# Kernel optimization log

Measured on AMD Instinct MI355X. Metric: run time of the kernel, lower is better.

Reference implementation:

```python
import jax, jax.numpy as jnp
import numpy as np

EPS = 1e-3  # Keras BatchNormalization default epsilon


def _binarize(x):
    # sign() binarization with straight-through estimator (identity gradient)
    b = jnp.where(x >= 0, 1.0, -1.0).astype(x.dtype)
    return x + jax.lax.stop_gradient(b - x)


def _conv(x, w):
    # NHWC input, HWIO kernel, stride 1, 'same' padding
    return jax.lax.conv_general_dilated(
        x, w, (1, 1), 'SAME', dimension_numbers=('NHWC', 'HWIO', 'NHWC'))


def _bn(x, p):
    # p: [4, C] rows = gamma, beta, moving_mean, moving_var (inference BN)
    gamma, beta, mean, var = p[0], p[1], p[2], p[3]
    return gamma * (x - mean) * jax.lax.rsqrt(var + EPS) + beta


def _maxpool(x):
    return jax.lax.reduce_window(x, -jnp.inf, jax.lax.max,
                                 (1, 2, 2, 1), (1, 2, 2, 1), 'VALID')


def _bconv_block(x, w, bn_p):
    # BinaryConv2D(activation='relu', use_bias=False) -> BatchNormalization
    y = jax.nn.relu(_conv(_binarize(x), _binarize(w)))
    return _bn(y, bn_p)


def setup_inputs() -> dict:
    key = jax.random.key(0)
    ks = iter(jax.random.split(key, 64))

    def w(shape, scale=0.05):
        return jax.random.normal(next(ks), shape, jnp.float32) * scale

    def bn_params(c):
        gamma = 1.0 + 0.1 * jax.random.normal(next(ks), (c,), jnp.float32)
        beta = 0.1 * jax.random.normal(next(ks), (c,), jnp.float32)
        mean = 0.1 * jax.random.normal(next(ks), (c,), jnp.float32)
        var = 0.5 + jax.random.uniform(next(ks), (c,), jnp.float32)
        return jnp.stack([gamma, beta, mean, var])

    inp = {
        'inputs': jax.random.normal(next(ks), (16, 224, 224, 3), jnp.float32),
        'conv1_w': w((3, 3, 3, 64)), 'conv1_b': w((64,)), 'bn1': bn_params(64),
        'w2': w((3, 3, 64, 128)),  'bn2': bn_params(128),
        'w3': w((3, 3, 128, 256)), 'bn3': bn_params(256),
        'w4': w((3, 3, 256, 256)), 'bn4': bn_params(256),
        'w5': w((3, 3, 256, 512)), 'bn5': bn_params(512),
        'w6': w((3, 3, 512, 512)), 'bn6': bn_params(512),
        'w7': w((3, 3, 512, 512)), 'bn7': bn_params(512),
        'w8': w((3, 3, 512, 512)), 'bn8': bn_params(512),
        'dense_w': w((512, 1000)),
    }
    return inp


def reference(inputs, conv1_w, conv1_b, bn1, w2, bn2, w3, bn3, w4, bn4,
              w5, bn5, w6, bn6, w7, bn7, w8, bn8, dense_w):
    # stage 1: full-precision conv -> BN -> maxpool
    x = jax.nn.relu(_conv(inputs, conv1_w) + conv1_b)
    x = _bn(x, bn1)
    x = _maxpool(x)              # 224 -> 112
    x = 0.5 * x                  # Scale(0.5)
    # binary (XNOR) conv stages, stride 1 (use_maxpool=True)
    x = _bconv_block(x, w2, bn2)
    x = _maxpool(x)              # 112 -> 56
    x = _bconv_block(x, w3, bn3)
    x = _bconv_block(x, w4, bn4)
    x = _maxpool(x)              # 56 -> 28
    x = _bconv_block(x, w5, bn5)
    x = _bconv_block(x, w6, bn6)
    x = _maxpool(x)              # 28 -> 14
    x = _bconv_block(x, w7, bn7)
    x = _bconv_block(x, w8, bn8)
    x = _maxpool(x)              # 14 -> 7
    x = jnp.mean(x, axis=(1, 2))  # global average pool -> [B, 512]
    # BinaryDense: binarized input and weights, no bias
    return _binarize(x) @ _binarize(dense_w)
```

## Files before the change

kernel.cpp:

```cpp
#include <hip/hip_runtime.h>
#include <cstdint>

using u64 = unsigned long long;

__global__ void pack_conv_weights(const float* __restrict__ w, u64* __restrict__ wb,
                                  int Cin, int Cout) {
    int cinw = Cin >> 6;
    int total = 9 * cinw * Cout;
    int idx = blockIdx.x * blockDim.x + threadIdx.x;
    if (idx >= total) return;
    int co = idx % Cout;
    int rest = idx / Cout;
    int wd = rest % cinw;
    int t = rest / cinw;
    u64 word = 0ull;
    for (int b = 0; b < 64; ++b) {
        int ci = (wd << 6) + b;
        float v = w[(t * Cin + ci) * Cout + co];
        if (v >= 0.f) word |= (1ull << b);
    }
    wb[idx] = word;
}

__global__ void pack_dense_weights(const float* __restrict__ w, u64* __restrict__ wb) {
    int j = blockIdx.x * blockDim.x + threadIdx.x;
    if (j >= 1000) return;
    for (int wd = 0; wd < 8; ++wd) {
        u64 word = 0ull;
        for (int b = 0; b < 64; ++b) {
            float v = w[((wd << 6) + b) * 1000 + j];
            if (v >= 0.f) word |= (1ull << b);
        }
        wb[j * 8 + wd] = word;
    }
}

__global__ void prep_bnthr(const float* __restrict__ bn, int cout,
                           double* __restrict__ thrd, int* __restrict__ sflag) {
    int i = blockIdx.x * blockDim.x + threadIdx.x;
    if (i >= cout) return;
    double g  = (double)bn[i];
    double be = (double)bn[cout + i];
    double mu = (double)bn[2 * cout + i];
    double va = (double)bn[3 * cout + i];
    double s  = g * (1.0 / sqrt(va + 1e-3));
    thrd[i] = mu - be / s;
    sflag[i] = (s >= 0.0) ? 1 : 0;
}

__global__ void prep_thrf(const double* __restrict__ thrd, float* __restrict__ thrf) {
    int i = threadIdx.x;
    if (i < 64) thrf[i] = (float)thrd[i];
}

__global__ __launch_bounds__(256, 1)
void conv1_fused(const float* __restrict__ in, const float* __restrict__ w,
                 const float* __restrict__ bias,
                 const float* __restrict__ thrf, const double* __restrict__ thrd,
                 const int* __restrict__ sflag,
                 u64* __restrict__ outbits) {
    int lane = threadIdx.x & 63;
    int wid = blockIdx.x * (blockDim.x >> 6) + (threadIdx.x >> 6);
    int pxq = wid % 28;
    int py  = (wid / 28) % 112;
    int n   = wid / (28 * 112);

    float  thrv = thrf[lane];
    double thrD = thrd[lane];
    bool   spos = (sflag[lane] != 0);
    float  bif  = bias[lane];

    float wreg[27];
#pragma unroll
    for (int t = 0; t < 9; ++t)
#pragma unroll
        for (int c = 0; c < 3; ++c)
            wreg[t * 3 + c] = w[(t * 3 + c) * 64 + lane];

    const float TAU = 2e-4f;
    int iy0 = 2 * py - 1;
    bool rowint = (py >= 1) & (py <= 110);

#pragma unroll 1
    for (int pp = 0; pp < 4; ++pp) {
        int px = 4 * pxq + pp;
        int ix0 = 2 * px - 1;

        float patch[4][12];
        bool interior = rowint & (px >= 1) & (px <= 110);
        if (interior) {
            const float* base = in + ((size_t)(n * 224 + iy0) * 224 + ix0) * 3;
#pragma unroll
            for (int r = 0; r < 4; ++r) {
                const float* rp = base + (size_t)r * (224 * 3);
#pragma unroll
                for (int c = 0; c < 12; ++c) patch[r][c] = rp[c];
            }
        } else {
#pragma unroll
            for (int r = 0; r < 4; ++r) {
                int iy = iy0 + r;
                bool rv = (iy >= 0) & (iy < 224);
#pragma unroll
                for (int cc = 0; cc < 4; ++cc) {
                    int ix = ix0 + cc;
                    bool v = rv & (ix >= 0) & (ix < 224);
                    const float* p = in + ((size_t)(n * 224 + iy) * 224 + ix) * 3;
#pragma unroll
                    for (int c = 0; c < 3; ++c)
                        patch[r][cc * 3 + c] = v ? p[c] : 0.f;
                }
            }
        }

        bool pred = false;
#pragma unroll
        for (int q = 0; q < 4; ++q) {
            int qy = q >> 1, qx = q & 1;
            float accf = bif;
#pragma unroll
            for (int dy = 0; dy < 3; ++dy)
#pragma unroll
                for (int dx = 0; dx < 3; ++dx)
#pragma unroll
                    for (int c = 0; c < 3; ++c)
                        accf = fmaf(patch[qy + dy][(qx + dx) * 3 + c],
                                    wreg[(dy * 3 + dx) * 3 + c], accf);
            float rf = fmaxf(accf, 0.f);
            bool p = spos ? (rf >= thrv) : (rf <= thrv);
            if (fabsf(rf - thrv) < TAU) {
                double acc = (double)bif;
#pragma unroll
                for (int dy = 0; dy < 3; ++dy)
#pragma unroll
                    for (int dx = 0; dx < 3; ++dx)
#pragma unroll
                        for (int c = 0; c < 3; ++c)
                            acc = fma((double)patch[qy + dy][(qx + dx) * 3 + c],
                                      (double)wreg[(dy * 3 + dx) * 3 + c], acc);
                double rd = fmax(acc, 0.0);
                p = spos ? (rd >= thrD) : (rd <= thrD);
            }
            pred |= p;
        }
        u64 word = __ballot(pred);
        if (lane == 0) outbits[((size_t)(n * 112 + py)) * 112 + px] = word;
    }
}

template<int CINW, int COUT, int P, bool OUTF64>
__global__ void bconv(const u64* __restrict__ xin, const u64* __restrict__ wb,
                      const float* __restrict__ bn,
                      const double* __restrict__ thrd, const int* __restrict__ sflag,
                      u64* __restrict__ obits, double* __restrict__ of64,
                      int H, int W) {
    constexpr int CW = COUT >> 6;
    __shared__ u64 sh[3][P + 2][CINW];

    int tid = threadIdx.x;
    int XT = (W + P - 1) / P;
    int pos = blockIdx.x;
    int xt = pos % XT;
    int yy = (pos / XT) % H;
    int n  = pos / (XT * H);
    int x0 = xt * P;

    for (int i = tid; i < 3 * (P + 2) * CINW; i += COUT) {
        int wd = i % CINW;
        int cc = (i / CINW) % (P + 2);
        int rr = i / (CINW * (P + 2));
        int gy = yy - 1 + rr, gx = x0 - 1 + cc;
        u64 v = 0ull;
        if (gy >= 0 && gy < H && gx >= 0 && gx < W)
            v = xin[((size_t)(n * H + gy) * W + gx) * CINW + wd];
        sh[rr][cc][wd] = v;
    }
    __syncthreads();

    int acc[P], nv[P];
#pragma unroll
    for (int p = 0; p < P; ++p) { acc[p] = 0; nv[p] = 0; }

    int co = tid;
    for (int dy = 0; dy < 3; ++dy) {
        int gy = yy - 1 + dy;
        if (gy < 0 || gy >= H) continue;
        for (int dx = 0; dx < 3; ++dx) {
            u64 wreg[CINW];
#pragma unroll
            for (int w = 0; w < CINW; ++w)
                wreg[w] = wb[((dy * 3 + dx) * CINW + w) * COUT + co];
#pragma unroll
            for (int p = 0; p < P; ++p) {
                int gx = x0 + p + dx - 1;
                if (gx >= 0 && gx < W) {
                    nv[p]++;
#pragma unroll
                    for (int w = 0; w < CINW; ++w)
                        acc[p] += __popcll(sh[dy][p + dx][w] ^ wreg[w]);
                }
            }
        }
    }

    int lane = tid & 63, wv = tid >> 6;

    if constexpr (OUTF64) {
        double g  = (double)bn[co];
        double be = (double)bn[COUT + co];
        double mu = (double)bn[2 * COUT + co];
        double va = (double)bn[3 * COUT + co];
        double rsq = 1.0 / sqrt(va + 1e-3);
        for (int p = 0; p < P; ++p) {
            int x = x0 + p;
            int y = nv[p] * (CINW * 64) - 2 * acc[p];
            int yr = y > 0 ? y : 0;
            double v = g * ((double)yr - mu) * rsq + be;
            if (x < W) of64[((size_t)(n * H + yy) * W + x) * COUT + co] = v;
        }
    } else {
        double thr = thrd[co];
        bool spos = (sflag[co] != 0);
        for (int p = 0; p < P; ++p) {
            int x = x0 + p;
            int y = nv[p] * (CINW * 64) - 2 * acc[p];
            int yr = y > 0 ? y : 0;
            double yd = (double)yr;
            bool pred = spos ? (yd >= thr) : (yd <= thr);
            u64 word = __ballot(pred);
            if (lane == 0 && x < W)
                obits[((size_t)(n * H + yy) * W + x) * CW + wv] = word;
        }
    }
}

__global__ void pool_bits(const u64* __restrict__ in, u64* __restrict__ out,
                          int H2, int W2, int CW) {
    int idx = blockIdx.x * blockDim.x + threadIdx.x;
    int total = 16 * H2 * W2 * CW;
    if (idx >= total) return;
    int wd = idx % CW;
    int rest = idx / CW;
    int px = rest % W2; rest /= W2;
    int py = rest % H2;
    int n = rest / H2;
    int W = 2 * W2;
    const u64* base = in + ((size_t)(n * 2 * H2 + 2 * py) * W + 2 * px) * CW + wd;
    out[idx] = base[0] | base[CW] | base[(size_t)W * CW] | base[(size_t)W * CW + CW];
}

__global__ void gap_binarize(const double* __restrict__ x, u64* __restrict__ gb) {
    int n = blockIdx.x;
    int co = threadIdx.x;
    double sum = 0.0;
    for (int py = 0; py < 7; ++py) {
        for (int px = 0; px < 7; ++px) {
            const double* b = x + ((size_t)(n * 14 + 2 * py) * 14 + 2 * px) * 512 + co;
            double m = b[0];
            m = fmax(m, b[512]);
            m = fmax(m, b[14 * 512]);
            m = fmax(m, b[14 * 512 + 512]);
            sum += m;
        }
    }
    double mean = sum / 49.0;
    bool pred = (mean >= 0.0);
    u64 word = __ballot(pred);
    if ((co & 63) == 0) gb[n * 8 + (co >> 6)] = word;
}

__global__ void dense_bin(const u64* __restrict__ gb, const u64* __restrict__ dwb,
                          float* __restrict__ out) {
    int idx = blockIdx.x * blockDim.x + threadIdx.x;
    if (idx >= 16000) return;
    int j = idx % 1000, n = idx / 1000;
    const u64* g = gb + n * 8;
    const u64* w = dwb + j * 8;
    int acc = 0;
#pragma unroll
    for (int wd = 0; wd < 8; ++wd) acc += __popcll(g[wd] ^ w[wd]);
    out[idx] = (float)(512 - 2 * acc);
}

extern "C" void kernel_launch(void* const* d_in, const int* in_sizes, int n_in,
                              void* d_out, int out_size, void* d_ws, size_t ws_size,
                              hipStream_t stream) {
    const float* inputs = (const float*)d_in[0];
    const float* w1  = (const float*)d_in[1];
    const float* b1  = (const float*)d_in[2];
    const float* bn1 = (const float*)d_in[3];
    const float* w2  = (const float*)d_in[4];
    const float* bn2 = (const float*)d_in[5];
    const float* w3  = (const float*)d_in[6];
    const float* bn3 = (const float*)d_in[7];
    const float* w4  = (const float*)d_in[8];
    const float* bn4 = (const float*)d_in[9];
    const float* w5  = (const float*)d_in[10];
    const float* bn5 = (const float*)d_in[11];
    const float* w6  = (const float*)d_in[12];
    const float* bn6 = (const float*)d_in[13];
    const float* w7  = (const float*)d_in[14];
    const float* bn7 = (const float*)d_in[15];
    const float* w8  = (const float*)d_in[16];
    const float* bn8 = (const float*)d_in[17];
    const float* dw  = (const float*)d_in[18];
    float* out = (float*)d_out;

    u64* ws = (u64*)d_ws;
    size_t o = 0;
    auto alloc = [&](size_t n) { u64* p = ws + o; o += n; return p; };

    u64* wb2 = alloc(9 * 1 * 128);
    u64* wb3 = alloc(9 * 2 * 256);
    u64* wb4 = alloc(9 * 4 * 256);
    u64* wb5 = alloc(9 * 4 * 512);
    u64* wb6 = alloc(9 * 8 * 512);
    u64* wb7 = alloc(9 * 8 * 512);
    u64* wb8 = alloc(9 * 8 * 512);
    u64* dwb = alloc(1000 * 8);

    double* th1 = (double*)alloc(64);   int* sf1 = (int*)alloc(64);
    double* th2 = (double*)alloc(128);  int* sf2 = (int*)alloc(128);
    double* th3 = (double*)alloc(256);  int* sf3 = (int*)alloc(256);
    double* th4 = (double*)alloc(256);  int* sf4 = (int*)alloc(256);
    double* th5 = (double*)alloc(512);  int* sf5 = (int*)alloc(512);
    double* th6 = (double*)alloc(512);  int* sf6 = (int*)alloc(512);
    double* th7 = (double*)alloc(512);  int* sf7 = (int*)alloc(512);
    float*  tf1 = (float*)alloc(64);

    u64* x2b = alloc(16 * 112 * 112 * 1);
    u64* c2b = alloc(16 * 112 * 112 * 2);
    u64* x3b = alloc(16 * 56 * 56 * 2);
    u64* c3b = alloc(16 * 56 * 56 * 4);
    u64* c4b = alloc(16 * 56 * 56 * 4);
    u64* x5b = alloc(16 * 28 * 28 * 4);
    u64* c5b = alloc(16 * 28 * 28 * 8);
    u64* c6b = alloc(16 * 28 * 28 * 8);
    u64* x7b = alloc(16 * 14 * 14 * 8);
    u64* c7b = alloc(16 * 14 * 14 * 8);
    u64* gb  = alloc(16 * 8);
    double* c8f = (double*)alloc(16 * 14 * 14 * 512);

    auto grid = [](int n, int b) { return (n + b - 1) / b; };
    pack_conv_weights<<<grid(9 * 1 * 128, 256), 256, 0, stream>>>(w2, wb2, 64, 128);
    pack_conv_weights<<<grid(9 * 2 * 256, 256), 256, 0, stream>>>(w3, wb3, 128, 256);
    pack_conv_weights<<<grid(9 * 4 * 256, 256), 256, 0, stream>>>(w4, wb4, 256, 256);
    pack_conv_weights<<<grid(9 * 4 * 512, 256), 256, 0, stream>>>(w5, wb5, 256, 512);
    pack_conv_weights<<<grid(9 * 8 * 512, 256), 256, 0, stream>>>(w6, wb6, 512, 512);
    pack_conv_weights<<<grid(9 * 8 * 512, 256), 256, 0, stream>>>(w7, wb7, 512, 512);
    pack_conv_weights<<<grid(9 * 8 * 512, 256), 256, 0, stream>>>(w8, wb8, 512, 512);
    pack_dense_weights<<<4, 256, 0, stream>>>(dw, dwb);

    prep_bnthr<<<1, 64, 0, stream>>>(bn1, 64, th1, sf1);
    prep_bnthr<<<1, 128, 0, stream>>>(bn2, 128, th2, sf2);
    prep_bnthr<<<1, 256, 0, stream>>>(bn3, 256, th3, sf3);
    prep_bnthr<<<1, 256, 0, stream>>>(bn4, 256, th4, sf4);
    prep_bnthr<<<grid(512, 256), 256, 0, stream>>>(bn5, 512, th5, sf5);
    prep_bnthr<<<grid(512, 256), 256, 0, stream>>>(bn6, 512, th6, sf6);
    prep_bnthr<<<grid(512, 256), 256, 0, stream>>>(bn7, 512, th7, sf7);
    prep_thrf<<<1, 64, 0, stream>>>(th1, tf1);

    conv1_fused<<<16 * 112 * 28 / 4, 256, 0, stream>>>(inputs, w1, b1, tf1, th1, sf1, x2b);

    bconv<1, 128, 8, false><<<16 * 112 * 14, 128, 0, stream>>>(x2b, wb2, bn2, th2, sf2, c2b, nullptr, 112, 112);
    pool_bits<<<grid(16 * 56 * 56 * 2, 256), 256, 0, stream>>>(c2b, x3b, 56, 56, 2);
    bconv<2, 256, 8, false><<<16 * 56 * 7, 256, 0, stream>>>(x3b, wb3, bn3, th3, sf3, c3b, nullptr, 56, 56);
    bconv<4, 256, 8, false><<<16 * 56 * 7, 256, 0, stream>>>(c3b, wb4, bn4, th4, sf4, c4b, nullptr, 56, 56);
    pool_bits<<<grid(16 * 28 * 28 * 4, 256), 256, 0, stream>>>(c4b, x5b, 28, 28, 4);
    bconv<4, 512, 7, false><<<16 * 28 * 4, 512, 0, stream>>>(x5b, wb5, bn5, th5, sf5, c5b, nullptr, 28, 28);
    bconv<8, 512, 7, false><<<16 * 28 * 4, 512, 0, stream>>>(c5b, wb6, bn6, th6, sf6, c6b, nullptr, 28, 28);
    pool_bits<<<grid(16 * 14 * 14 * 8, 256), 256, 0, stream>>>(c6b, x7b, 14, 14, 8);
    bconv<8, 512, 7, false><<<16 * 14 * 2, 512, 0, stream>>>(x7b, wb7, bn7, th7, sf7, c7b, nullptr, 14, 14);
    bconv<8, 512, 7, true><<<16 * 14 * 2, 512, 0, stream>>>(c7b, wb8, bn8, nullptr, nullptr, nullptr, c8f, 14, 14);

    gap_binarize<<<16, 512, 0, stream>>>(c8f, gb);
    dense_bin<<<grid(16000, 256), 256, 0, stream>>>(gb, dwb, out);
}
```

Measured before the change: 526.7 us.

## Restructure binary conv inner loop to reuse each shared word across three taps

The binary conv inner loop now walks over input words and columns, loading each shared-memory word once and XOR-popcounting it against the three horizontal-tap weights. Previously each shared word was reloaded for every tap. Per-pixel valid-tap counts are now derived analytically from edge flags instead of being counted at runtime. The global-average-pool reduction is split into a parallel partial-sum kernel plus a small final kernel, so more blocks run in parallel at the cost of an extra launch. The non-unrolled loop over weight words trades register pressure for less unrolling.

```diff
diff --git a/kernel.cpp b/kernel.cpp
--- a/kernel.cpp
+++ b/kernel.cpp
@@ -177,32 +177,35 @@
     }
     __syncthreads();
 
-    int acc[P], nv[P];
-#pragma unroll
-    for (int p = 0; p < P; ++p) { acc[p] = 0; nv[p] = 0; }
+    int acc[P];
+#pragma unroll
+    for (int p = 0; p < P; ++p) acc[p] = 0;
 
     int co = tid;
+    bool leftv  = (x0 > 0);
+    bool rightv = (x0 + P < W);
+
     for (int dy = 0; dy < 3; ++dy) {
         int gy = yy - 1 + dy;
         if (gy < 0 || gy >= H) continue;
-        for (int dx = 0; dx < 3; ++dx) {
-            u64 wreg[CINW];
-#pragma unroll
-            for (int w = 0; w < CINW; ++w)
-                wreg[w] = wb[((dy * 3 + dx) * CINW + w) * COUT + co];
-#pragma unroll
-            for (int p = 0; p < P; ++p) {
-                int gx = x0 + p + dx - 1;
-                if (gx >= 0 && gx < W) {
-                    nv[p]++;
-#pragma unroll
-                    for (int w = 0; w < CINW; ++w)
-                        acc[p] += __popcll(sh[dy][p + dx][w] ^ wreg[w]);
-                }
+#pragma unroll 1
+        for (int w = 0; w < CINW; ++w) {
+            u64 w0 = wb[((dy * 3 + 0) * CINW + w) * COUT + co];
+            u64 w1 = wb[((dy * 3 + 1) * CINW + w) * COUT + co];
+            u64 w2 = wb[((dy * 3 + 2) * CINW + w) * COUT + co];
+#pragma unroll
+            for (int c = 0; c < P + 2; ++c) {
+                if (c == 0 && !leftv) continue;
+                if (c == P + 1 && !rightv) continue;
+                u64 v = sh[dy][c][w];
+                if (c < P)  acc[c]     += __popcll(v ^ w0);
+                if (c >= 1 && c <= P) acc[c - 1] += __popcll(v ^ w1);
+                if (c >= 2) acc[c - 2] += __popcll(v ^ w2);
             }
         }
     }
 
+    int ndy = 3 - (yy == 0) - (yy == H - 1);
     int lane = tid & 63, wv = tid >> 6;
 
     if constexpr (OUTF64) {
@@ -211,9 +214,12 @@
         double mu = (double)bn[2 * COUT + co];
         double va = (double)bn[3 * COUT + co];
         double rsq = 1.0 / sqrt(va + 1e-3);
+#pragma unroll
         for (int p = 0; p < P; ++p) {
             int x = x0 + p;
-            int y = nv[p] * (CINW * 64) - 2 * acc[p];
+            bool eL = (x == 0), eR = (x == W - 1);
+            int nvp = ndy * (3 - eL - eR);
+            int y = nvp * (CINW * 64) - 2 * acc[p];
             int yr = y > 0 ? y : 0;
             double v = g * ((double)yr - mu) * rsq + be;
             if (x < W) of64[((size_t)(n * H + yy) * W + x) * COUT + co] = v;
@@ -221,9 +227,12 @@
     } else {
         double thr = thrd[co];
         bool spos = (sflag[co] != 0);
+#pragma unroll
         for (int p = 0; p < P; ++p) {
             int x = x0 + p;
-            int y = nv[p] * (CINW * 64) - 2 * acc[p];
+            bool eL = (x == 0), eR = (x == W - 1);
+            int nvp = ndy * (3 - eL - eR);
+            int y = nvp * (CINW * 64) - 2 * acc[p];
             int yr = y > 0 ? y : 0;
             double yd = (double)yr;
             bool pred = spos ? (yd >= thr) : (yd <= thr);
@@ -249,20 +258,27 @@
     out[idx] = base[0] | base[CW] | base[(size_t)W * CW] | base[(size_t)W * CW + CW];
 }
 
-__global__ void gap_binarize(const double* __restrict__ x, u64* __restrict__ gb) {
+__global__ void gap_part(const double* __restrict__ x, double* __restrict__ part) {
+    int b = blockIdx.x;
+    int py = b % 7, n = b / 7;
+    int co = threadIdx.x;
+    double sum = 0.0;
+    for (int px = 0; px < 7; ++px) {
+        const double* bp = x + ((size_t)(n * 14 + 2 * py) * 14 + 2 * px) * 512 + co;
+        double m = bp[0];
+        m = fmax(m, bp[512]);
+        m = fmax(m, bp[14 * 512]);
+        m = fmax(m, bp[14 * 512 + 512]);
+        sum += m;
+    }
+    part[((size_t)n * 7 + py) * 512 + co] = sum;
+}
+
+__global__ void gap_final(const double* __restrict__ part, u64* __restrict__ gb) {
     int n = blockIdx.x;
     int co = threadIdx.x;
     double sum = 0.0;
-    for (int py = 0; py < 7; ++py) {
-        for (int px = 0; px < 7; ++px) {
-            const double* b = x + ((size_t)(n * 14 + 2 * py) * 14 + 2 * px) * 512 + co;
-            double m = b[0];
-            m = fmax(m, b[512]);
-            m = fmax(m, b[14 * 512]);
-            m = fmax(m, b[14 * 512 + 512]);
-            sum += m;
-        }
-    }
+    for (int py = 0; py < 7; ++py) sum += part[((size_t)n * 7 + py) * 512 + co];
     double mean = sum / 49.0;
     bool pred = (mean >= 0.0);
     u64 word = __ballot(pred);
@@ -339,7 +355,8 @@
     u64* x7b = alloc(16 * 14 * 14 * 8);
     u64* c7b = alloc(16 * 14 * 14 * 8);
     u64* gb  = alloc(16 * 8);
-    double* c8f = (double*)alloc(16 * 14 * 14 * 512);
+    double* c8f   = (double*)alloc(16 * 14 * 14 * 512);
+    double* gpart = (double*)alloc(16 * 7 * 512);
 
     auto grid = [](int n, int b) { return (n + b - 1) / b; };
     pack_conv_weights<<<grid(9 * 1 * 128, 256), 256, 0, stream>>>(w2, wb2, 64, 128);
@@ -373,6 +390,7 @@
     bconv<8, 512, 7, false><<<16 * 14 * 2, 512, 0, stream>>>(x7b, wb7, bn7, th7, sf7, c7b, nullptr, 14, 14);
     bconv<8, 512, 7, true><<<16 * 14 * 2, 512, 0, stream>>>(c7b, wb8, bn8, nullptr, nullptr, nullptr, c8f, 14, 14);
 
-    gap_binarize<<<16, 512, 0, stream>>>(c8f, gb);
+    gap_part<<<16 * 7, 512, 0, stream>>>(c8f, gpart);
+    gap_final<<<16, 512, 0, stream>>>(gpart, gb);
     dense_bin<<<grid(16000, 256), 256, 0, stream>>>(gb, dwb, out);
 }
```

After: 518.4 us. Within noise of the previous version (-1.6%).
